# Optimization experiments

Measured on AMD Instinct MI355X. Metric: run time of the kernel, lower is better.

## Reference

```python
import jax, jax.numpy as jnp
import numpy as np

N_NODES = 100000
N_EDGES = 1600000
IN_DIM, HID_DIM, OUT_DIM, N_CLASSES = 128, 256, 256, 200
N_GRAPHS = 64


def gcn_conv(x, edge_index, W, b):
    """PyG GCNConv: add self-loops, symmetric deg^{-1/2} normalization,
    aggregate source->target, then bias. Linear transform applied first
    (cheaper since in/out dims comparable)."""
    N = x.shape[0]
    loop = jnp.arange(N, dtype=edge_index.dtype)
    src = jnp.concatenate([edge_index[0], loop])
    dst = jnp.concatenate([edge_index[1], loop])
    deg = jax.ops.segment_sum(jnp.ones_like(dst, dtype=x.dtype), dst, num_segments=N)
    dinv = jnp.where(deg > 0, jax.lax.rsqrt(deg), 0.0)
    xw = x @ W  # [N, F_out]
    norm = dinv[src] * dinv[dst]  # [E+N]
    msg = xw[src] * norm[:, None]  # gather + scale
    out = jax.ops.segment_sum(msg, dst, num_segments=N)  # scatter-add
    return out + b


def global_mean_pool(x, batch, num_graphs):
    sums = jax.ops.segment_sum(x, batch, num_segments=num_graphs)
    cnt = jax.ops.segment_sum(jnp.ones((x.shape[0],), x.dtype), batch, num_segments=num_graphs)
    return sums / jnp.maximum(cnt, 1.0)[:, None]


def setup_inputs() -> dict:
    key = jax.random.key(0)
    ks = jax.random.split(key, 8)
    x = jax.random.normal(ks[0], (N_NODES, IN_DIM), dtype=jnp.float32)
    edge_index = jax.random.randint(ks[1], (2, N_EDGES), 0, N_NODES, dtype=jnp.int32)
    batch = jnp.sort(jax.random.randint(ks[2], (N_NODES,), 0, N_GRAPHS, dtype=jnp.int32))
    # Glorot-style init for weights (scaled normals)
    W1 = jax.random.normal(ks[3], (IN_DIM, HID_DIM), dtype=jnp.float32) / np.sqrt(IN_DIM)
    b1 = jnp.zeros((HID_DIM,), jnp.float32)
    W2 = jax.random.normal(ks[4], (HID_DIM, OUT_DIM), dtype=jnp.float32) / np.sqrt(HID_DIM)
    b2 = jnp.zeros((OUT_DIM,), jnp.float32)
    Wc = jax.random.normal(ks[5], (OUT_DIM, N_CLASSES), dtype=jnp.float32) / np.sqrt(OUT_DIM)
    bc = jnp.zeros((N_CLASSES,), jnp.float32)
    return {"x": x, "edge_index": edge_index, "batch": batch, "num_graphs": N_GRAPHS,
            "W1": W1, "b1": b1, "W2": W2, "b2": b2, "Wc": Wc, "bc": bc}


def reference(x, edge_index, batch, num_graphs, W1, b1, W2, b2, Wc, bc):
    h = jax.nn.relu(gcn_conv(x, edge_index, W1, b1))
    # dropout p=0.5 is identity in eval mode
    h = jax.nn.relu(gcn_conv(h, edge_index, W2, b2))
    g = global_mean_pool(h, batch, num_graphs)  # [num_graphs, OUT_DIM]
    return g @ Wc + bc  # [num_graphs, N_CLASSES]
```

## Files before the change

### kernel.cpp

```cpp
#include <hip/hip_runtime.h>
#include <cstdint>
#include <cstddef>


typedef __attribute__((ext_vector_type(8))) short bf16x8;
typedef __attribute__((ext_vector_type(4))) float f32x4;

#define P1_CHUNK 4096
#define BCAP 8192

__device__ inline unsigned short f2bf(float f) {
    unsigned u = __float_as_uint(f);
    u = (u + 0x7FFFu + ((u >> 16) & 1u)) >> 16;
    return (unsigned short)u;
}
__device__ inline unsigned nib4(unsigned u) {
    return (u & 15u) | (((u >> 8) & 15u) << 4) | (((u >> 16) & 15u) << 8) |
           (((u >> 24) & 15u) << 12);
}

__global__ __launch_bounds__(256) void bucket_scatter_kernel(
        const int* __restrict__ src, const int* __restrict__ dst,
        int* __restrict__ bucketCnt, unsigned long long* __restrict__ pairs,
        int E, int NB) {
    __shared__ int hist[512];
    __shared__ int base[512];
    int t = threadIdx.x;
    int e0 = blockIdx.x * P1_CHUNK;
    int eend = min(e0 + P1_CHUNK, E);
    for (int i = t; i < NB; i += 256) hist[i] = 0;
    __syncthreads();
    for (int e = e0 + t; e < eend; e += 256) atomicAdd(&hist[dst[e] >> 8], 1);
    __syncthreads();
    for (int i = t; i < NB; i += 256) {
        int c = hist[i];
        base[i] = (c > 0) ? atomicAdd(&bucketCnt[i], c) : 0;
        hist[i] = 0;
    }
    __syncthreads();
    for (int e = e0 + t; e < eend; e += 256) {
        int d = dst[e], s = src[e];
        int b = d >> 8;
        int r = base[b] + atomicAdd(&hist[b], 1);
        if (r < BCAP)
            pairs[(size_t)b * BCAP + r] =
                (unsigned long long)(unsigned)s | ((unsigned long long)(d & 255) << 32);
    }
}

__global__ __launch_bounds__(256) void fine_place_kernel(
        const unsigned long long* __restrict__ pairs, const int* __restrict__ bucketCnt,
        int* __restrict__ off, float* __restrict__ dinv, int* __restrict__ csr,
        int N, int E) {
    __shared__ int hist[256];
    __shared__ int loff[256];
    __shared__ int ws[4];
    __shared__ int sbase;
    int b = blockIdx.x, t = threadIdx.x;
    int lane = t & 63, w = t >> 6;

    int part = 0;
    for (int i = t; i < b; i += 256) part += bucketCnt[i];
    #pragma unroll
    for (int d = 1; d < 64; d <<= 1) part += __shfl_xor(part, d, 64);
    if (lane == 0) ws[w] = part;
    __syncthreads();
    if (t == 0) sbase = ws[0] + ws[1] + ws[2] + ws[3];
    if (b == 0 && t == 0) off[N] = E;
    __syncthreads();
    int base = sbase;

    int cnt = min(bucketCnt[b], BCAP);
    const unsigned long long* pp = pairs + (size_t)b * BCAP;
    hist[t] = 0;
    __syncthreads();
    for (int i = t; i < cnt; i += 256) atomicAdd(&hist[(int)(pp[i] >> 32)], 1);
    __syncthreads();
    int v = hist[t];
    {
        int x = v;
        #pragma unroll
        for (int d = 1; d < 64; d <<= 1) {
            int y = __shfl_up(x, d, 64);
            if (lane >= d) x += y;
        }
        if (lane == 63) ws[w] = x;
        __syncthreads();
        int woff = 0;
        #pragma unroll
        for (int j = 0; j < 4; j++)
            if (j < w) woff += ws[j];
        loff[t] = woff + x - v;
    }
    int node = b * 256 + t;
    if (node < N) {
        off[node] = base + loff[t];
        dinv[node] = rsqrtf((float)v + 1.0f);
    }
    __syncthreads();
    hist[t] = 0;
    __syncthreads();
    for (int i = t; i < cnt; i += 256) {
        unsigned long long pr = pp[i];
        int dl = (int)(pr >> 32);
        int r = atomicAdd(&hist[dl], 1);
        csr[base + loff[dl] + r] = (int)(unsigned)pr;
    }
}

__global__ __launch_bounds__(256) void prep1_kernel(
        const float* __restrict__ W1, unsigned short* __restrict__ WT1, int K1,
        const float* __restrict__ W2, unsigned short* __restrict__ WT2,
        const int* __restrict__ batch, int* __restrict__ cnt, int N) {
    __shared__ int h[256];
    int bid = blockIdx.x, t = threadIdx.x;
    if (bid < K1) {
        int idx = bid * 256 + t;
        int k = idx >> 8, n = idx & 255;
        WT1[n * K1 + k] = f2bf(W1[idx]);
    } else if (bid < K1 + 256) {
        int idx = (bid - K1) * 256 + t;
        int k = idx >> 8, n = idx & 255;
        WT2[n * 256 + k] = f2bf(W2[idx]);
    } else {
        h[t] = 0;
        __syncthreads();
        int n = (bid - K1 - 256) * 256 + t;
        if (n < N) atomicAdd(&h[batch[n]], 1);
        __syncthreads();
        if (h[t] != 0) atomicAdd(&cnt[t], h[t]);
    }
}

__global__ __launch_bounds__(256) void prescale_q8_kernel(
        const float* __restrict__ x, const float* __restrict__ dinv,
        unsigned short* __restrict__ Q, float* __restrict__ scale, int N) {
    int node = blockIdx.x * 4 + (threadIdx.x >> 6);
    int lane = threadIdx.x & 63;
    if (node >= N) return;
    float2 v = reinterpret_cast<const float2*>(x)[(size_t)node * 64 + lane];
    float m = fmaxf(fabsf(v.x), fabsf(v.y));
    #pragma unroll
    for (int d = 32; d >= 1; d >>= 1) m = fmaxf(m, __shfl_xor(m, d, 64));
    float qinv = m > 0.f ? 127.f / m : 0.f;
    int q0 = (int)rintf(v.x * qinv), q1 = (int)rintf(v.y * qinv);
    Q[(size_t)node * 64 + lane] = (unsigned short)((q0 & 255) | ((q1 & 255) << 8));
    if (lane == 0) scale[node] = dinv[node] * m * (1.f / 127.f);
}

__global__ __launch_bounds__(256) void aggregate_q8_kernel(
        const unsigned short* __restrict__ Q, const float* __restrict__ scale,
        unsigned short* __restrict__ OUT,
        const int* __restrict__ off, const int* __restrict__ csr,
        const float* __restrict__ dinv, int N) {
    int node = __builtin_amdgcn_readfirstlane(blockIdx.x * 4 + (threadIdx.x >> 6));
    int lane = threadIdx.x & 63;
    if (node >= N) return;

    float acc[2];
    auto loadpay = [&](int s) -> unsigned {
        return (unsigned)Q[(size_t)s * 64 + lane];
    };
    auto dec = [&](unsigned v, int q) -> float {
        return (float)(int)(signed char)(v >> (8 * q));
    };
    {
        unsigned v = loadpay(node);
        float sc = scale[node];
        acc[0] = sc * dec(v, 0);
        acc[1] = sc * dec(v, 1);
    }
    int e0 = off[node], e1 = off[node + 1];
    int e = e0;
    for (; e + 16 <= e1; e += 16) {
        int s[16]; unsigned v[16]; float sc[16];
        #pragma unroll
        for (int j = 0; j < 16; j++) s[j] = csr[e + j];
        #pragma unroll
        for (int j = 0; j < 16; j++) { v[j] = loadpay(s[j]); sc[j] = scale[s[j]]; }
        #pragma unroll
        for (int j = 0; j < 16; j++) { acc[0] += sc[j] * dec(v[j], 0); acc[1] += sc[j] * dec(v[j], 1); }
    }
    if (e + 8 <= e1) {
        int s[8]; unsigned v[8]; float sc[8];
        #pragma unroll
        for (int j = 0; j < 8; j++) s[j] = csr[e + j];
        #pragma unroll
        for (int j = 0; j < 8; j++) { v[j] = loadpay(s[j]); sc[j] = scale[s[j]]; }
        #pragma unroll
        for (int j = 0; j < 8; j++) { acc[0] += sc[j] * dec(v[j], 0); acc[1] += sc[j] * dec(v[j], 1); }
        e += 8;
    }
    for (; e < e1; e++) {
        int s = csr[e];
        unsigned v = loadpay(s);
        float sc = scale[s];
        acc[0] += sc * dec(v, 0); acc[1] += sc * dec(v, 1);
    }
    float di = dinv[node];
    unsigned o = (unsigned)f2bf(di * acc[0]) | ((unsigned)f2bf(di * acc[1]) << 16);
    reinterpret_cast<unsigned*>(OUT)[(size_t)node * 64 + lane] = o;
}

__global__ __launch_bounds__(256) void aggregate_q4_kernel(
        const unsigned short* __restrict__ Q4, const float* __restrict__ scale,
        unsigned short* __restrict__ OUT,
        const int* __restrict__ off, const int* __restrict__ csr,
        const float* __restrict__ dinv, int N) {
    int node = __builtin_amdgcn_readfirstlane(blockIdx.x * 4 + (threadIdx.x >> 6));
    int lane = threadIdx.x & 63;
    if (node >= N) return;

    float acc[4];
    auto loadpay = [&](int s) -> unsigned {
        return (unsigned)Q4[(size_t)s * 64 + lane];
    };
    auto dec = [&](unsigned h, int q) -> float {
        return (float)((h >> (4 * q)) & 15u);
    };
    {
        unsigned v = loadpay(node);
        float sc = scale[node];
        #pragma unroll
        for (int q = 0; q < 4; q++) acc[q] = sc * dec(v, q);
    }
    int e0 = off[node], e1 = off[node + 1];
    int e = e0;
    for (; e + 16 <= e1; e += 16) {
        int s[16]; unsigned v[16]; float sc[16];
        #pragma unroll
        for (int j = 0; j < 16; j++) s[j] = csr[e + j];
        #pragma unroll
        for (int j = 0; j < 16; j++) { v[j] = loadpay(s[j]); sc[j] = scale[s[j]]; }
        #pragma unroll
        for (int j = 0; j < 16; j++)
            #pragma unroll
            for (int q = 0; q < 4; q++) acc[q] += sc[j] * dec(v[j], q);
    }
    if (e + 8 <= e1) {
        int s[8]; unsigned v[8]; float sc[8];
        #pragma unroll
        for (int j = 0; j < 8; j++) s[j] = csr[e + j];
        #pragma unroll
        for (int j = 0; j < 8; j++) { v[j] = loadpay(s[j]); sc[j] = scale[s[j]]; }
        #pragma unroll
        for (int j = 0; j < 8; j++)
            #pragma unroll
            for (int q = 0; q < 4; q++) acc[q] += sc[j] * dec(v[j], q);
        e += 8;
    }
    for (; e < e1; e++) {
        int s = csr[e];
        unsigned v = loadpay(s);
        float sc = scale[s];
        #pragma unroll
        for (int q = 0; q < 4; q++) acc[q] += sc * dec(v, q);
    }
    float di = dinv[node];
    uint2 o;
    o.x = (unsigned)f2bf(di * acc[0]) | ((unsigned)f2bf(di * acc[1]) << 16);
    o.y = (unsigned)f2bf(di * acc[2]) | ((unsigned)f2bf(di * acc[3]) << 16);
    reinterpret_cast<uint2*>(OUT)[(size_t)node * 64 + lane] = o;
}

template <int K, int MODE>
__global__ __launch_bounds__(256) void mfma_gemm_kernel(
        const unsigned short* __restrict__ A, const unsigned short* __restrict__ WT,
        const float* __restrict__ bias, const float* __restrict__ dinv,
        char* __restrict__ Cq, float* __restrict__ scaleOut,
        const int* __restrict__ batch, float* __restrict__ gsum, int M, int ntiles) {
    constexpr int KK = K / 32;
    constexpr int RB = K * 2;
    constexpr int CHUNKS = 64 * RB / 16;
    constexpr int EXTRA = (MODE == 0) ? (256 * 4 + 64 * 4 + 64 * 256) : (4 * 256 * 4);
    __shared__ __align__(16) char Abuf[2][64 * RB];
    __shared__ __align__(16) char extra[EXTRA];

    const int t = threadIdx.x;
    const int lane = t & 63, w = t >> 6;
    const int lhi = lane >> 4, l15 = lane & 15;

    bf16x8 breg[4][KK];
    #pragma unroll
    for (int nf = 0; nf < 4; nf++)
        #pragma unroll
        for (int kk = 0; kk < KK; kk++)
            breg[nf][kk] = *reinterpret_cast<const bf16x8*>(
                WT + (size_t)(w * 64 + nf * 16 + l15) * K + kk * 32 + lhi * 8);
    float bn[4];
    #pragma unroll
    for (int nf = 0; nf < 4; nf++) bn[nf] = bias[w * 64 + nf * 16 + l15];

    auto stage = [&](char* dstbuf, int tile) {
        int r0 = tile * 64;
        #pragma unroll
        for (int p = 0; p < CHUNKS / 256; p++) {
            int idx = p * 256 + t;
            int row = idx / (RB / 16);
            int cb = idx % (RB / 16);
            int sbyte = (cb * 16) ^ ((row & 7) << 4);
            const char* g = (const char*)(A + (size_t)(r0 + row) * K) + sbyte;
            __builtin_amdgcn_global_load_lds(
                (const __attribute__((address_space(1))) void*)g,
                (__attribute__((address_space(3))) void*)(dstbuf + idx * 16),
                16, 0, 0);
        }
    };

    int tile = blockIdx.x;
    if (tile >= ntiles) return;
    stage(Abuf[0], tile);
    __syncthreads();
    int c = 0;

    for (; tile < ntiles; tile += gridDim.x) {
        int nxt = tile + gridDim.x;
        if (nxt < ntiles) stage(Abuf[c ^ 1], nxt);

        f32x4 acc[4][4];
        #pragma unroll
        for (int i = 0; i < 4; i++)
            #pragma unroll
            for (int j = 0; j < 4; j++) acc[i][j] = (f32x4){0.f, 0.f, 0.f, 0.f};

        const char* buf = Abuf[c];
        #pragma unroll
        for (int kk = 0; kk < KK; kk++) {
            bf16x8 a[4];
            int kb = (kk * 32 + lhi * 8) * 2;
            #pragma unroll
            for (int mf = 0; mf < 4; mf++) {
                int row = mf * 16 + l15;
                a[mf] = *reinterpret_cast<const bf16x8*>(
                    buf + row * RB + (kb ^ ((row & 7) << 4)));
            }
            #pragma unroll
            for (int mf = 0; mf < 4; mf++)
                #pragma unroll
                for (int nf = 0; nf < 4; nf++)
                    acc[mf][nf] = __builtin_amdgcn_mfma_f32_16x16x32_bf16(
                        a[mf], breg[nf][kk], acc[mf][nf], 0, 0, 0);
        }

        int r0 = tile * 64;
        if constexpr (MODE == 0) {
            float* wmax = (float*)extra;
            float* qinv = wmax + 256;
            char* pack = (char*)(qinv + 64);
            #pragma unroll
            for (int mf = 0; mf < 4; mf++)
                #pragma unroll
                for (int j = 0; j < 4; j++) {
                    float lmax = 0.f;
                    #pragma unroll
                    for (int nf = 0; nf < 4; nf++) {
                        float v = fmaxf(acc[mf][nf][j] + bn[nf], 0.f);
                        acc[mf][nf][j] = v;
                        lmax = fmaxf(lmax, v);
                    }
                    lmax = fmaxf(lmax, __shfl_xor(lmax, 1, 64));
                    lmax = fmaxf(lmax, __shfl_xor(lmax, 2, 64));
                    lmax = fmaxf(lmax, __shfl_xor(lmax, 4, 64));
                    lmax = fmaxf(lmax, __shfl_xor(lmax, 8, 64));
                    if (l15 == 0) wmax[w * 64 + mf * 16 + lhi * 4 + j] = lmax;
                }
            __syncthreads();
            if (t < 64) {
                float m4 = fmaxf(fmaxf(wmax[t], wmax[64 + t]),
                                 fmaxf(wmax[128 + t], wmax[192 + t]));
                qinv[t] = m4 > 0.f ? 15.f / m4 : 0.f;
                if (r0 + t < M) scaleOut[r0 + t] = dinv[r0 + t] * m4 * (1.f / 15.f);
            }
            __syncthreads();
            #pragma unroll
            for (int mf = 0; mf < 4; mf++)
                #pragma unroll
                for (int j = 0; j < 4; j++) {
                    int r = mf * 16 + lhi * 4 + j;
                    float qi = qinv[r];
                    #pragma unroll
                    for (int nf = 0; nf < 4; nf++)
                        pack[r * 256 + w * 64 + nf * 16 + l15] =
                            (char)min((int)rintf(acc[mf][nf][j] * qi), 15);
                }
            __syncthreads();
            #pragma unroll
            for (int p = 0; p < 4; p++) {
                int idx = p * 256 + t;
                uint4 s4 = reinterpret_cast<const uint4*>(pack)[idx];
                uint2 o;
                o.x = nib4(s4.x) | (nib4(s4.y) << 16);
                o.y = nib4(s4.z) | (nib4(s4.w) << 16);
                reinterpret_cast<uint2*>(Cq + (size_t)r0 * 128)[idx] = o;
            }
        } else {
            float* psum = (float*)extra;
            int gmin = batch[min(r0, M - 1)];
            int gmax = batch[min(r0 + 63, M - 1)];
            if (gmin == gmax) {
                #pragma unroll
                for (int nf = 0; nf < 4; nf++) {
                    float s = 0.f;
                    #pragma unroll
                    for (int mf = 0; mf < 4; mf++)
                        #pragma unroll
                        for (int j = 0; j < 4; j++) {
                            int m = r0 + mf * 16 + lhi * 4 + j;
                            float v = fmaxf(acc[mf][nf][j] + bn[nf], 0.f);
                            s += (m < M) ? v : 0.f;
                        }
                    psum[lhi * 256 + w * 64 + nf * 16 + l15] = s;
                }
                __syncthreads();
                float tot = psum[t] + psum[256 + t] + psum[512 + t] + psum[768 + t];
                atomicAdd(&gsum[(size_t)gmin * 256 + t], tot);
            } else {
                #pragma unroll
                for (int mf = 0; mf < 4; mf++)
                    #pragma unroll
                    for (int j = 0; j < 4; j++) {
                        int m = r0 + mf * 16 + lhi * 4 + j;
                        if (m < M) {
                            int g = batch[m];
                            #pragma unroll
                            for (int nf = 0; nf < 4; nf++)
                                atomicAdd(&gsum[(size_t)g * 256 + w * 64 + nf * 16 + l15],
                                          fmaxf(acc[mf][nf][j] + bn[nf], 0.f));
                        }
                    }
            }
        }
        __syncthreads();
        c ^= 1;
    }
}


__global__ __launch_bounds__(256) void pool_final_kernel(const float* __restrict__ gsum,
                                                         const int* __restrict__ cnt,
                                                         const float* __restrict__ Wc,
                                                         const float* __restrict__ bc,
                                                         float* __restrict__ out) {
    __shared__ float gm[256];
    int g = blockIdx.x, t = threadIdx.x;
    float inv = 1.0f / fmaxf((float)cnt[g], 1.0f);
    gm[t] = gsum[g * 256 + t] * inv;
    __syncthreads();
    if (t < 200) {
        float acc = bc[t];
        #pragma unroll 8
        for (int k = 0; k < 256; k++) acc += gm[k] * Wc[k * 200 + t];
        out[g * 200 + t] = acc;
    }
}


extern "C" void kernel_launch(void* const* d_in, const int* in_sizes, int n_in,
                              void* d_out, int out_size, void* d_ws, size_t ws_size,
                              hipStream_t stream) {
    const float* x   = (const float*)d_in[0];
    const int* ei    = (const int*)d_in[1];
    const int* batch = (const int*)d_in[2];
    const float* W1  = (const float*)d_in[4];
    const float* b1  = (const float*)d_in[5];
    const float* W2  = (const float*)d_in[6];
    const float* b2  = (const float*)d_in[7];
    const float* Wc  = (const float*)d_in[8];
    const float* bc  = (const float*)d_in[9];
    float* out = (float*)d_out;

    const int N = in_sizes[2];
    const int E = in_sizes[1] / 2;
    const int G = out_size / 200;
    const int K1 = in_sizes[0] / N;
    const int Mpad = (N + 63) & ~63;
    const int NB = (N + 255) >> 8;
    const int ntiles = Mpad / 64;
    const int* src = ei;
    const int* dst = ei + E;

    char* p = (char*)d_ws;
    auto alloc = [&](size_t bytes) -> char* {
        char* r = p;
        p += (bytes + 255) & ~(size_t)255;
        return r;
    };
    int*   off    = (int*)alloc((size_t)(N + 1) * 4);
    int*   bktCnt = (int*)alloc((size_t)NB * 4);
    int*   cnt    = (int*)alloc(256 * 4);
    float* dinv   = (float*)alloc((size_t)N * 4);
    float* scale0 = (float*)alloc((size_t)N * 4);
    float* scale1 = (float*)alloc((size_t)N * 4);
    float* gsum   = (float*)alloc((size_t)G * 256 * 4);
    int*   csr    = (int*)alloc((size_t)E * 4);
    unsigned long long* pairs = (unsigned long long*)alloc((size_t)NB * BCAP * 8);
    unsigned short* WT1 = (unsigned short*)alloc((size_t)256 * K1 * 2);
    unsigned short* WT2 = (unsigned short*)alloc((size_t)256 * 256 * 2);
    unsigned short* Y0q  = (unsigned short*)alloc((size_t)N * K1);
    char*           Y1q4 = alloc((size_t)Mpad * 128);
    unsigned short* a1   = (unsigned short*)alloc((size_t)Mpad * K1 * 2);
    unsigned short* a2   = (unsigned short*)alloc((size_t)Mpad * 256 * 2);

    hipMemsetAsync(bktCnt, 0, (size_t)NB * 4, stream);
    hipMemsetAsync(cnt, 0, 256 * 4, stream);
    hipMemsetAsync(gsum, 0, (size_t)G * 256 * 4, stream);

    int blkN = (N + 255) / 256;
    bucket_scatter_kernel<<<(E + P1_CHUNK - 1) / P1_CHUNK, 256, 0, stream>>>(
        src, dst, bktCnt, pairs, E, NB);
    prep1_kernel<<<K1 + 256 + blkN, 256, 0, stream>>>(W1, WT1, K1, W2, WT2, batch, cnt, N);
    fine_place_kernel<<<NB, 256, 0, stream>>>(pairs, bktCnt, off, dinv, csr, N, E);
    prescale_q8_kernel<<<(N + 3) / 4, 256, 0, stream>>>(x, dinv, Y0q, scale0, N);

    aggregate_q8_kernel<<<(N + 3) / 4, 256, 0, stream>>>(Y0q, scale0, a1, off, csr, dinv, N);
    mfma_gemm_kernel<128, 0><<<768, 256, 0, stream>>>(
        a1, WT1, b1, dinv, Y1q4, scale1, nullptr, nullptr, N, ntiles);
    aggregate_q4_kernel<<<(N + 3) / 4, 256, 0, stream>>>(
        (const unsigned short*)Y1q4, scale1, a2, off, csr, dinv, N);
    mfma_gemm_kernel<256, 1><<<512, 256, 0, stream>>>(
        a2, WT2, b2, nullptr, nullptr, nullptr, batch, gsum, N, ntiles);
    pool_final_kernel<<<G, 256, 0, stream>>>(gsum, cnt, Wc, bc, out);
}
```

Baseline: 326.7 us.

## Pack edge pairs into 32 bits and launch one GEMM tile per block

Bucket pairs are now 32-bit words, with the source node in the low 24 bits and the local destination in the high 8, which halves the scatter and fine-place traffic. The MFMA GEMM kernels drop the persistent double-buffered tile loop and launch one block per 64-row tile with a single LDS buffer. This frees LDS and may raise occupancy, but each block now reloads the weight fragments into registers. The pooling path replaces the shared-memory partial sum with wave shuffles plus per-wave atomics. Source ids must fit in 24 bits, which holds for 100k nodes.

```diff
diff --git a/kernel.cpp b/kernel.cpp
--- a/kernel.cpp
+++ b/kernel.cpp
@@ -21,7 +21,7 @@
 
 __global__ __launch_bounds__(256) void bucket_scatter_kernel(
         const int* __restrict__ src, const int* __restrict__ dst,
-        int* __restrict__ bucketCnt, unsigned long long* __restrict__ pairs,
+        int* __restrict__ bucketCnt, unsigned* __restrict__ pairs,
         int E, int NB) {
     __shared__ int hist[512];
     __shared__ int base[512];
@@ -43,13 +43,12 @@
         int b = d >> 8;
         int r = base[b] + atomicAdd(&hist[b], 1);
         if (r < BCAP)
-            pairs[(size_t)b * BCAP + r] =
-                (unsigned long long)(unsigned)s | ((unsigned long long)(d & 255) << 32);
+            pairs[(size_t)b * BCAP + r] = (unsigned)s | ((unsigned)(d & 255) << 24);
     }
 }
 
 __global__ __launch_bounds__(256) void fine_place_kernel(
-        const unsigned long long* __restrict__ pairs, const int* __restrict__ bucketCnt,
+        const unsigned* __restrict__ pairs, const int* __restrict__ bucketCnt,
         int* __restrict__ off, float* __restrict__ dinv, int* __restrict__ csr,
         int N, int E) {
     __shared__ int hist[256];
@@ -71,10 +70,10 @@
     int base = sbase;
 
     int cnt = min(bucketCnt[b], BCAP);
-    const unsigned long long* pp = pairs + (size_t)b * BCAP;
+    const unsigned* pp = pairs + (size_t)b * BCAP;
     hist[t] = 0;
     __syncthreads();
-    for (int i = t; i < cnt; i += 256) atomicAdd(&hist[(int)(pp[i] >> 32)], 1);
+    for (int i = t; i < cnt; i += 256) atomicAdd(&hist[pp[i] >> 24], 1);
     __syncthreads();
     int v = hist[t];
     {
@@ -101,10 +100,10 @@
     hist[t] = 0;
     __syncthreads();
     for (int i = t; i < cnt; i += 256) {
-        unsigned long long pr = pp[i];
-        int dl = (int)(pr >> 32);
+        unsigned pr = pp[i];
+        int dl = pr >> 24;
         int r = atomicAdd(&hist[dl], 1);
-        csr[base + loff[dl] + r] = (int)(unsigned)pr;
+        csr[base + loff[dl] + r] = (int)(pr & 0xFFFFFFu);
     }
 }
 
@@ -268,17 +267,19 @@
         const unsigned short* __restrict__ A, const unsigned short* __restrict__ WT,
         const float* __restrict__ bias, const float* __restrict__ dinv,
         char* __restrict__ Cq, float* __restrict__ scaleOut,
-        const int* __restrict__ batch, float* __restrict__ gsum, int M, int ntiles) {
+        const int* __restrict__ batch, float* __restrict__ gsum, int M) {
     constexpr int KK = K / 32;
     constexpr int RB = K * 2;
     constexpr int CHUNKS = 64 * RB / 16;
-    constexpr int EXTRA = (MODE == 0) ? (256 * 4 + 64 * 4 + 64 * 256) : (4 * 256 * 4);
-    __shared__ __align__(16) char Abuf[2][64 * RB];
+    constexpr int EXTRA = (MODE == 0) ? (256 * 4 + 64 * 4 + 64 * 256) : 16;
+    __shared__ __align__(16) char As[64 * RB];
     __shared__ __align__(16) char extra[EXTRA];
 
     const int t = threadIdx.x;
     const int lane = t & 63, w = t >> 6;
     const int lhi = lane >> 4, l15 = lane & 15;
+    const int tile = blockIdx.x;
+    const int r0 = tile * 64;
 
     bf16x8 breg[4][KK];
     #pragma unroll
@@ -291,147 +292,129 @@
     #pragma unroll
     for (int nf = 0; nf < 4; nf++) bn[nf] = bias[w * 64 + nf * 16 + l15];
 
-    auto stage = [&](char* dstbuf, int tile) {
-        int r0 = tile * 64;
-        #pragma unroll
-        for (int p = 0; p < CHUNKS / 256; p++) {
-            int idx = p * 256 + t;
-            int row = idx / (RB / 16);
-            int cb = idx % (RB / 16);
-            int sbyte = (cb * 16) ^ ((row & 7) << 4);
-            const char* g = (const char*)(A + (size_t)(r0 + row) * K) + sbyte;
-            __builtin_amdgcn_global_load_lds(
-                (const __attribute__((address_space(1))) void*)g,
-                (__attribute__((address_space(3))) void*)(dstbuf + idx * 16),
-                16, 0, 0);
+    #pragma unroll
+    for (int p = 0; p < CHUNKS / 256; p++) {
+        int idx = p * 256 + t;
+        int row = idx / (RB / 16);
+        int cb = idx % (RB / 16);
+        int sbyte = (cb * 16) ^ ((row & 7) << 4);
+        const char* g = (const char*)(A + (size_t)(r0 + row) * K) + sbyte;
+        __builtin_amdgcn_global_load_lds(
+            (const __attribute__((address_space(1))) void*)g,
+            (__attribute__((address_space(3))) void*)(As + idx * 16),
+            16, 0, 0);
+    }
+    __syncthreads();
+
+    f32x4 acc[4][4];
+    #pragma unroll
+    for (int i = 0; i < 4; i++)
+        #pragma unroll
+        for (int j = 0; j < 4; j++) acc[i][j] = (f32x4){0.f, 0.f, 0.f, 0.f};
+
+    #pragma unroll
+    for (int kk = 0; kk < KK; kk++) {
+        bf16x8 a[4];
+        int kb = (kk * 32 + lhi * 8) * 2;
+        #pragma unroll
+        for (int mf = 0; mf < 4; mf++) {
+            int row = mf * 16 + l15;
+            a[mf] = *reinterpret_cast<const bf16x8*>(
+                As + row * RB + (kb ^ ((row & 7) << 4)));
         }
-    };
-
-    int tile = blockIdx.x;
-    if (tile >= ntiles) return;
-    stage(Abuf[0], tile);
-    __syncthreads();
-    int c = 0;
-
-    for (; tile < ntiles; tile += gridDim.x) {
-        int nxt = tile + gridDim.x;
-        if (nxt < ntiles) stage(Abuf[c ^ 1], nxt);
-
-        f32x4 acc[4][4];
-        #pragma unroll
-        for (int i = 0; i < 4; i++)
-            #pragma unroll
-            for (int j = 0; j < 4; j++) acc[i][j] = (f32x4){0.f, 0.f, 0.f, 0.f};
-
-        const char* buf = Abuf[c];
-        #pragma unroll
-        for (int kk = 0; kk < KK; kk++) {
-            bf16x8 a[4];
-            int kb = (kk * 32 + lhi * 8) * 2;
-            #pragma unroll
-            for (int mf = 0; mf < 4; mf++) {
-                int row = mf * 16 + l15;
-                a[mf] = *reinterpret_cast<const bf16x8*>(
-                    buf + row * RB + (kb ^ ((row & 7) << 4)));
+        #pragma unroll
+        for (int mf = 0; mf < 4; mf++)
+            #pragma unroll
+            for (int nf = 0; nf < 4; nf++)
+                acc[mf][nf] = __builtin_amdgcn_mfma_f32_16x16x32_bf16(
+                    a[mf], breg[nf][kk], acc[mf][nf], 0, 0, 0);
+    }
+
+    if constexpr (MODE == 0) {
+        float* wmax = (float*)extra;
+        float* qinv = wmax + 256;
+        char* pack = (char*)(qinv + 64);
+        #pragma unroll
+        for (int mf = 0; mf < 4; mf++)
+            #pragma unroll
+            for (int j = 0; j < 4; j++) {
+                float lmax = 0.f;
+                #pragma unroll
+                for (int nf = 0; nf < 4; nf++) {
+                    float v = fmaxf(acc[mf][nf][j] + bn[nf], 0.f);
+                    acc[mf][nf][j] = v;
+                    lmax = fmaxf(lmax, v);
+                }
+                lmax = fmaxf(lmax, __shfl_xor(lmax, 1, 64));
+                lmax = fmaxf(lmax, __shfl_xor(lmax, 2, 64));
+                lmax = fmaxf(lmax, __shfl_xor(lmax, 4, 64));
+                lmax = fmaxf(lmax, __shfl_xor(lmax, 8, 64));
+                if (l15 == 0) wmax[w * 64 + mf * 16 + lhi * 4 + j] = lmax;
             }
-            #pragma unroll
-            for (int mf = 0; mf < 4; mf++)
+        __syncthreads();
+        if (t < 64) {
+            float m4 = fmaxf(fmaxf(wmax[t], wmax[64 + t]),
+                             fmaxf(wmax[128 + t], wmax[192 + t]));
+            qinv[t] = m4 > 0.f ? 15.f / m4 : 0.f;
+            if (r0 + t < M) scaleOut[r0 + t] = dinv[r0 + t] * m4 * (1.f / 15.f);
+        }
+        __syncthreads();
+        #pragma unroll
+        for (int mf = 0; mf < 4; mf++)
+            #pragma unroll
+            for (int j = 0; j < 4; j++) {
+                int r = mf * 16 + lhi * 4 + j;
+                float qi = qinv[r];
                 #pragma unroll
                 for (int nf = 0; nf < 4; nf++)
-                    acc[mf][nf] = __builtin_amdgcn_mfma_f32_16x16x32_bf16(
-                        a[mf], breg[nf][kk], acc[mf][nf], 0, 0, 0);
+                    pack[r * 256 + w * 64 + nf * 16 + l15] =
+                        (char)min((int)rintf(acc[mf][nf][j] * qi), 15);
+            }
+        __syncthreads();
+        #pragma unroll
+        for (int p = 0; p < 4; p++) {
+            int idx = p * 256 + t;
+            uint4 s4 = reinterpret_cast<const uint4*>(pack)[idx];
+            uint2 o;
+            o.x = nib4(s4.x) | (nib4(s4.y) << 16);
+            o.y = nib4(s4.z) | (nib4(s4.w) << 16);
+            reinterpret_cast<uint2*>(Cq + (size_t)r0 * 128)[idx] = o;
         }
-
-        int r0 = tile * 64;
-        if constexpr (MODE == 0) {
-            float* wmax = (float*)extra;
-            float* qinv = wmax + 256;
-            char* pack = (char*)(qinv + 64);
-            #pragma unroll
-            for (int mf = 0; mf < 4; mf++)
-                #pragma unroll
-                for (int j = 0; j < 4; j++) {
-                    float lmax = 0.f;
-                    #pragma unroll
-                    for (int nf = 0; nf < 4; nf++) {
-                        float v = fmaxf(acc[mf][nf][j] + bn[nf], 0.f);
-                        acc[mf][nf][j] = v;
-                        lmax = fmaxf(lmax, v);
-                    }
-                    lmax = fmaxf(lmax, __shfl_xor(lmax, 1, 64));
-                    lmax = fmaxf(lmax, __shfl_xor(lmax, 2, 64));
-                    lmax = fmaxf(lmax, __shfl_xor(lmax, 4, 64));
-                    lmax = fmaxf(lmax, __shfl_xor(lmax, 8, 64));
-                    if (l15 == 0) wmax[w * 64 + mf * 16 + lhi * 4 + j] = lmax;
-                }
-            __syncthreads();
-            if (t < 64) {
-                float m4 = fmaxf(fmaxf(wmax[t], wmax[64 + t]),
-                                 fmaxf(wmax[128 + t], wmax[192 + t]));
-                qinv[t] = m4 > 0.f ? 15.f / m4 : 0.f;
-                if (r0 + t < M) scaleOut[r0 + t] = dinv[r0 + t] * m4 * (1.f / 15.f);
-            }
-            __syncthreads();
-            #pragma unroll
-            for (int mf = 0; mf < 4; mf++)
-                #pragma unroll
-                for (int j = 0; j < 4; j++) {
-                    int r = mf * 16 + lhi * 4 + j;
-                    float qi = qinv[r];
-                    #pragma unroll
-                    for (int nf = 0; nf < 4; nf++)
-                        pack[r * 256 + w * 64 + nf * 16 + l15] =
-                            (char)min((int)rintf(acc[mf][nf][j] * qi), 15);
-                }
-            __syncthreads();
-            #pragma unroll
-            for (int p = 0; p < 4; p++) {
-                int idx = p * 256 + t;
-                uint4 s4 = reinterpret_cast<const uint4*>(pack)[idx];
-                uint2 o;
-                o.x = nib4(s4.x) | (nib4(s4.y) << 16);
-                o.y = nib4(s4.z) | (nib4(s4.w) << 16);
-                reinterpret_cast<uint2*>(Cq + (size_t)r0 * 128)[idx] = o;
-            }
-        } else {
-            float* psum = (float*)extra;
-            int gmin = batch[min(r0, M - 1)];
-            int gmax = batch[min(r0 + 63, M - 1)];
-            if (gmin == gmax) {
-                #pragma unroll
-                for (int nf = 0; nf < 4; nf++) {
-                    float s = 0.f;
-                    #pragma unroll
-                    for (int mf = 0; mf < 4; mf++)
-                        #pragma unroll
-                        for (int j = 0; j < 4; j++) {
-                            int m = r0 + mf * 16 + lhi * 4 + j;
-                            float v = fmaxf(acc[mf][nf][j] + bn[nf], 0.f);
-                            s += (m < M) ? v : 0.f;
-                        }
-                    psum[lhi * 256 + w * 64 + nf * 16 + l15] = s;
-                }
-                __syncthreads();
-                float tot = psum[t] + psum[256 + t] + psum[512 + t] + psum[768 + t];
-                atomicAdd(&gsum[(size_t)gmin * 256 + t], tot);
-            } else {
+    } else {
+        int gmin = batch[min(r0, M - 1)];
+        int gmax = batch[min(r0 + 63, M - 1)];
+        if (gmin == gmax) {
+            #pragma unroll
+            for (int nf = 0; nf < 4; nf++) {
+                float s = 0.f;
                 #pragma unroll
                 for (int mf = 0; mf < 4; mf++)
                     #pragma unroll
                     for (int j = 0; j < 4; j++) {
                         int m = r0 + mf * 16 + lhi * 4 + j;
-                        if (m < M) {
-                            int g = batch[m];
-                            #pragma unroll
-                            for (int nf = 0; nf < 4; nf++)
-                                atomicAdd(&gsum[(size_t)g * 256 + w * 64 + nf * 16 + l15],
-                                          fmaxf(acc[mf][nf][j] + bn[nf], 0.f));
-                        }
+                        float v = fmaxf(acc[mf][nf][j] + bn[nf], 0.f);
+                        s += (m < M) ? v : 0.f;
                     }
+                s += __shfl_xor(s, 16, 64);
+                s += __shfl_xor(s, 32, 64);
+                if (lhi == 0)
+                    atomicAdd(&gsum[(size_t)gmin * 256 + w * 64 + nf * 16 + l15], s);
             }
+        } else {
+            #pragma unroll
+            for (int mf = 0; mf < 4; mf++)
+                #pragma unroll
+                for (int j = 0; j < 4; j++) {
+                    int m = r0 + mf * 16 + lhi * 4 + j;
+                    if (m < M) {
+                        int g = batch[m];
+                        #pragma unroll
+                        for (int nf = 0; nf < 4; nf++)
+                            atomicAdd(&gsum[(size_t)g * 256 + w * 64 + nf * 16 + l15],
+                                      fmaxf(acc[mf][nf][j] + bn[nf], 0.f));
+                    }
+                }
         }
-        __syncthreads();
-        c ^= 1;
     }
 }
 
@@ -493,7 +476,7 @@
     float* scale1 = (float*)alloc((size_t)N * 4);
     float* gsum   = (float*)alloc((size_t)G * 256 * 4);
     int*   csr    = (int*)alloc((size_t)E * 4);
-    unsigned long long* pairs = (unsigned long long*)alloc((size_t)NB * BCAP * 8);
+    unsigned* pairs = (unsigned*)alloc((size_t)NB * BCAP * 4);
     unsigned short* WT1 = (unsigned short*)alloc((size_t)256 * K1 * 2);
     unsigned short* WT2 = (unsigned short*)alloc((size_t)256 * 256 * 2);
     unsigned short* Y0q  = (unsigned short*)alloc((size_t)N * K1);
@@ -513,11 +496,11 @@
     prescale_q8_kernel<<<(N + 3) / 4, 256, 0, stream>>>(x, dinv, Y0q, scale0, N);
 
     aggregate_q8_kernel<<<(N + 3) / 4, 256, 0, stream>>>(Y0q, scale0, a1, off, csr, dinv, N);
-    mfma_gemm_kernel<128, 0><<<768, 256, 0, stream>>>(
-        a1, WT1, b1, dinv, Y1q4, scale1, nullptr, nullptr, N, ntiles);
+    mfma_gemm_kernel<128, 0><<<ntiles, 256, 0, stream>>>(
+        a1, WT1, b1, dinv, Y1q4, scale1, nullptr, nullptr, N);
     aggregate_q4_kernel<<<(N + 3) / 4, 256, 0, stream>>>(
         (const unsigned short*)Y1q4, scale1, a2, off, csr, dinv, N);
-    mfma_gemm_kernel<256, 1><<<512, 256, 0, stream>>>(
-        a2, WT2, b2, nullptr, nullptr, nullptr, batch, gsum, N, ntiles);
+    mfma_gemm_kernel<256, 1><<<ntiles, 256, 0, stream>>>(
+        a2, WT2, b2, nullptr, nullptr, nullptr, batch, gsum, N);
     pool_final_kernel<<<G, 256, 0, stream>>>(gsum, cnt, Wc, bc, out);
 }
```

New measurement: 283.0 us. -13.4%, faster.
